# Kernel tuning notes

Measured on AMD Instinct MI355X. Metric: run time of the kernel, lower is better.

Reference implementation:

```python
import jax, jax.numpy as jnp
import numpy as np

NEG_SLOPE = 0.2  # PyG GATConv default negative_slope
NUM_GRAPHS = 64
N, E, F_IN = 50000, 800000, 128


def _gat(x, src, dst, W, a_s, a_d, b, concat):
    # PyG GATConv: h = x W (per head); e_ij = leaky_relu(a_s.h_j + a_d.h_i);
    # softmax over incoming edges of each dst node; out_i = sum_j alpha_ij h_j
    n = x.shape[0]
    H, C = a_s.shape
    h = (x @ W).reshape(n, H, C)                     # [N,H,C]
    es = jnp.einsum('nhc,hc->nh', h, a_s)            # [N,H]
    ed = jnp.einsum('nhc,hc->nh', h, a_d)
    e = jax.nn.leaky_relu(es[src] + ed[dst], NEG_SLOPE)   # [E,H]
    m = jax.ops.segment_max(e, dst, num_segments=n)       # per-dst max (stable softmax)
    ex = jnp.exp(e - m[dst])
    den = jax.ops.segment_sum(ex, dst, num_segments=n)
    alpha = ex / den[dst]                                 # [E,H]
    out = jax.ops.segment_sum(h[src] * alpha[:, :, None], dst, num_segments=n)  # [N,H,C]
    if concat:
        return out.reshape(n, H * C) + b
    return out.mean(axis=1) + b


def setup_inputs() -> dict:
    key = jax.random.key(0)
    ks = jax.random.split(key, 10)
    x = jax.random.normal(ks[0], (N, F_IN), jnp.float32)
    edge_index = jax.random.randint(ks[1], (2, E), 0, N, dtype=jnp.int64)
    batch = jnp.sort(jax.random.randint(ks[2], (N,), 0, NUM_GRAPHS, dtype=jnp.int64))
    s1 = 1.0 / np.sqrt(F_IN)
    s2 = 1.0 / np.sqrt(256)
    return {
        'x': x,
        'edge_index': edge_index,
        'batch': batch,
        'W1': jax.random.normal(ks[3], (F_IN, 256), jnp.float32) * s1,
        'a_src1': jax.random.normal(ks[4], (4, 64), jnp.float32) * s2,
        'a_dst1': jax.random.normal(ks[5], (4, 64), jnp.float32) * s2,
        'b1': jnp.zeros((256,), jnp.float32),
        'W2': jax.random.normal(ks[6], (256, 128), jnp.float32) * s2,
        'a_src2': jax.random.normal(ks[7], (1, 128), jnp.float32) * (1.0 / np.sqrt(128)),
        'a_dst2': jax.random.normal(ks[8], (1, 128), jnp.float32) * (1.0 / np.sqrt(128)),
        'b2': jnp.zeros((128,), jnp.float32),
        'fc_w': jax.random.normal(ks[9], (128, 10), jnp.float32) * (1.0 / np.sqrt(128)),
        'fc_b': jnp.zeros((10,), jnp.float32),
    }


def reference(x, edge_index, batch, W1, a_src1, a_dst1, b1, W2, a_src2, a_dst2, b2, fc_w, fc_b):
    n = x.shape[0]
    loop = jnp.arange(n, dtype=edge_index.dtype)  # PyG add_self_loops=True
    src = jnp.concatenate([edge_index[0], loop])
    dst = jnp.concatenate([edge_index[1], loop])
    h = jax.nn.elu(_gat(x, src, dst, W1, a_src1, a_dst1, b1, True))   # dropout: eval mode -> identity
    h = jax.nn.elu(_gat(h, src, dst, W2, a_src2, a_dst2, b2, False))
    pooled = jax.ops.segment_sum(h, batch, num_segments=NUM_GRAPHS)
    cnt = jax.ops.segment_sum(jnp.ones((n,), h.dtype), batch, num_segments=NUM_GRAPHS)
    pooled = pooled / jnp.maximum(cnt, 1.0)[:, None]
    logits = pooled @ fc_w + fc_b
    return jax.nn.log_softmax(logits, axis=1)
```

## Files before the change

kernel.cpp:

```cpp
#include <hip/hip_runtime.h>
#include <math.h>

#define N_NODES 50000
#define N_PAD   50048
#define N_EDGES 800000
#define E_TOT   (N_EDGES + N_NODES)
#define NG 64
#define CAP 48
#define NBKT 512
#define BNODES 98
#define RCAP 24
#define FILL_CHUNK 2048
#define GEMM1_BLOCKS 782
#define FILL_BLOCKS  391
#define PH1_TOTAL (GEMM1_BLOCKS + FILL_BLOCKS)
#define G2_NB 32

typedef short short8 __attribute__((ext_vector_type(8)));
typedef float floatx4 __attribute__((ext_vector_type(4)));
typedef float floatx2 __attribute__((ext_vector_type(2)));

__device__ inline short f2bf(float f) {
    union { float f; unsigned u; } v; v.f = f;
    unsigned r = v.u + 0x7fff + ((v.u >> 16) & 1);
    return (short)(r >> 16);
}

__device__ inline unsigned f2fp8(float f) {
    union { float f; unsigned u; } v; v.f = f;
    unsigned s = v.u & 0x80000000u;
    unsigned au = v.u & 0x7fffffffu;
    if (au > 0x43E00000u) au = 0x43E00000u;
    unsigned r = au + 0x7ffffu + ((au >> 20) & 1);
    int e8 = (int)(r >> 23) - 120;
    unsigned m3 = (r >> 20) & 7;
    unsigned code;
    if (e8 <= 0) code = 0;
    else if (e8 > 15) code = 0x7e;
    else code = ((unsigned)e8 << 3) | m3;
    return (s >> 24) | code;
}

__device__ inline float leaky_exp(float t) {
    t = t > 0.f ? t : 0.2f * t;
    return __expf(t);
}


__global__ __launch_bounds__(256) void phase1_kernel(const float* __restrict__ x,
                                                     const float* __restrict__ W1,
                                                     const float* __restrict__ a_s,
                                                     const float* __restrict__ a_d,
                                                     const int* __restrict__ ei,
                                                     unsigned short* __restrict__ gcnt,
                                                     unsigned* __restrict__ gb2,
                                                     unsigned char* __restrict__ C8,
                                                     float* __restrict__ es,
                                                     float* __restrict__ ed,
                                                     const float* __restrict__ W2,
                                                     const float* __restrict__ as2,
                                                     const float* __restrict__ ad2,
                                                     float* __restrict__ ws2,
                                                     float* __restrict__ wd2,
                                                     float* __restrict__ pooled) {
    __shared__ short bs[64][136];
    __shared__ int hist[NBKT];
    int bid = blockIdx.x;
    int tid = threadIdx.x;

    if (bid == PH1_TOTAL) {
        int k = tid;
        float s = 0.f, d = 0.f;
        for (int c = 0; c < 128; c++) {
            float w = W2[k * 128 + c];
            s += w * as2[c];
            d += w * ad2[c];
        }
        ws2[k] = s;
        wd2[k] = d;
        for (int i = tid; i < NG * 128; i += 256) pooled[i] = 0.f;
        return;
    }

    int gb = -1, fb = -1;
    {
        int g3 = bid / 3, r3 = bid - g3 * 3;
        if (r3 == 2) fb = g3;
        else         gb = g3 * 2 + r3;
    }

    if (fb >= 0) {
        hist[tid] = 0; hist[tid + 256] = 0;
        __syncthreads();
        unsigned meta[8], pay[8];
        int e0 = fb * FILL_CHUNK;
#pragma unroll
        for (int j = 0; j < 8; j++) {
            int t = e0 + j * 256 + tid;
            if (t < N_EDGES) {
                int s = ei[t];
                int d = ei[N_EDGES + t];
                unsigned bkt = (unsigned)d / 98u;
                int dlow = d - (int)bkt * 98;
                int pos = atomicAdd(&hist[bkt], 1);
                meta[j] = (bkt << 16) | (unsigned)pos;
                pay[j] = ((unsigned)s << 9) | (unsigned)dlow;
            } else {
                meta[j] = 0xffffffffu;
            }
        }
        __syncthreads();
        {
            int c0h = hist[tid];        if (c0h > RCAP) c0h = RCAP;
            int c1h = hist[tid + 256];  if (c1h > RCAP) c1h = RCAP;
            gcnt[fb * NBKT + tid] = (unsigned short)c0h;
            gcnt[fb * NBKT + tid + 256] = (unsigned short)c1h;
        }
#pragma unroll
        for (int j = 0; j < 8; j++) {
            if (meta[j] != 0xffffffffu) {
                unsigned bkt = meta[j] >> 16;
                unsigned pos = meta[j] & 0xffffu;
                if (pos < RCAP)
                    gb2[((size_t)bkt * FILL_BLOCKS + fb) * RCAP + pos] = pay[j];
            }
        }
        return;
    }

    const int K = 128, N = 256;
    int tc = tid & 63;
    int tk0s = (tid >> 6) * 32;
    int wid = tid >> 6;
    int lane = tid & 63;
    int m0 = gb * 64 + wid * 16;
    int mr = lane & 15;
    int quad = lane >> 4;
    int kq = quad << 3;
    int arow = m0 + mr; if (arow > N_NODES - 1) arow = N_NODES - 1;
    const float* aptr = x + (size_t)arow * K + kq;
    short8 a[4];
#pragma unroll
    for (int kk = 0; kk < 4; kk++) {
        float4 f0 = *(const float4*)(aptr + kk * 32);
        float4 f1 = *(const float4*)(aptr + kk * 32 + 4);
        a[kk][0] = f2bf(f0.x); a[kk][1] = f2bf(f0.y); a[kk][2] = f2bf(f0.z); a[kk][3] = f2bf(f0.w);
        a[kk][4] = f2bf(f1.x); a[kk][5] = f2bf(f1.y); a[kk][6] = f2bf(f1.z); a[kk][7] = f2bf(f1.w);
    }
    int orow = m0 + (quad << 2);
    for (int head = 0; head < 4; head++) {
        int c0 = head * 64;
        if (head) __syncthreads();
        for (int k = tk0s; k < tk0s + 32; k++)
            bs[tc][k] = f2bf(W1[k * 256 + c0 + tc]);
        __syncthreads();
        floatx4 acc[4] = {{0.f,0.f,0.f,0.f},{0.f,0.f,0.f,0.f},{0.f,0.f,0.f,0.f},{0.f,0.f,0.f,0.f}};
#pragma unroll
        for (int kk = 0; kk < 4; kk++) {
#pragma unroll
            for (int t = 0; t < 4; t++) {
                short8 b = *(const short8*)&bs[t * 16 + mr][kq + kk * 32];
                acc[t] = __builtin_amdgcn_mfma_f32_16x16x32_bf16(a[kk], b, acc[t], 0, 0, 0);
            }
        }
        float asv[4], adv[4];
#pragma unroll
        for (int t = 0; t < 4; t++) {
            asv[t] = a_s[c0 + t * 16 + mr];
            adv[t] = a_d[c0 + t * 16 + mr];
        }
#pragma unroll
        for (int r = 0; r < 4; r++) {
            float ps = acc[0][r] * asv[0] + acc[1][r] * asv[1] + acc[2][r] * asv[2] + acc[3][r] * asv[3];
            float pd = acc[0][r] * adv[0] + acc[1][r] * adv[1] + acc[2][r] * adv[2] + acc[3][r] * adv[3];
#pragma unroll
            for (int off = 8; off >= 1; off >>= 1) {
                ps += __shfl_xor(ps, off);
                pd += __shfl_xor(pd, off);
            }
            if (mr == 0) {
                es[(orow + r) * 4 + head] = ps;
                ed[(orow + r) * 4 + head] = pd;
            }
        }
#pragma unroll
        for (int t = 0; t < 4; t++) {
            int ocol = c0 + t * 16 + mr;
#pragma unroll
            for (int r = 0; r < 4; r++) {
                C8[(size_t)(orow + r) * N + ocol] = (unsigned char)f2fp8(acc[t][r]);
            }
        }
    }
}


__global__ __launch_bounds__(512) void binfill_kernel(const unsigned* __restrict__ gb2,
                                                      const unsigned short* __restrict__ gcnt,
                                                      unsigned short* __restrict__ col,
                                                      int* __restrict__ degT) {
    __shared__ unsigned colL[BNODES * CAP / 2];
    __shared__ int cnt[BNODES];
    __shared__ unsigned short cl[FILL_BLOCKS + 1];
    int b = blockIdx.x, tid = threadIdx.x;
    int nbase = b * BNODES;

    for (int i = tid; i < BNODES * CAP / 8; i += 512) ((uint4*)colL)[i] = make_uint4(0, 0, 0, 0);
    if (tid < FILL_BLOCKS) cl[tid] = gcnt[tid * NBKT + b];
    if (tid < BNODES) cnt[tid] = (nbase + tid < N_NODES) ? 1 : 0;
    __syncthreads();

    if (tid < BNODES) {
        int nn = nbase + tid;
        if (nn < N_NODES) ((unsigned short*)colL)[tid * CAP] = (unsigned short)nn;
    }
    const uint4* src4 = (const uint4*)(gb2 + (size_t)b * FILL_BLOCKS * RCAP);
    for (int r = tid; r < FILL_BLOCKS * RCAP / 4; r += 512) {
        int blk = r / 6;
        int q = r - blk * 6;
        int c = cl[blk];
        if (q * 4 < c) {
            uint4 v = src4[r];
            unsigned vv[4] = {v.x, v.y, v.z, v.w};
#pragma unroll
            for (int j = 0; j < 4; j++) {
                if (q * 4 + j < c) {
                    unsigned p = vv[j];
                    int dlow = (int)(p & 511u);
                    int s = (int)(p >> 9);
                    int sp = atomicAdd(&cnt[dlow], 1);
                    if (sp < CAP) ((unsigned short*)colL)[dlow * CAP + sp] = (unsigned short)s;
                }
            }
        }
    }
    __syncthreads();

    uint4* cb = (uint4*)(col + (size_t)b * BNODES * CAP);
    for (int i = tid; i < BNODES * CAP / 8; i += 512) cb[i] = ((uint4*)colL)[i];
    if (tid < BNODES) {
        int nn = nbase + tid;
        if (nn < N_NODES) degT[nn] = cnt[tid];
    }
}


__global__ __launch_bounds__(256) void gather1_kernel(const unsigned char* __restrict__ h8,
                                                      const int* __restrict__ degT,
                                                      const unsigned short* __restrict__ col,
                                                      const float* __restrict__ es,
                                                      const float* __restrict__ ed,
                                                      const float* __restrict__ bias,
                                                      const float* __restrict__ ws2,
                                                      const float* __restrict__ wd2,
                                                      short* __restrict__ out,
                                                      float* __restrict__ es2,
                                                      float* __restrict__ ed2) {
    __shared__ float wlds[4][CAP * 4];
    __shared__ unsigned short ilds[4][CAP];
    int tid = threadIdx.x;
    int wid = tid >> 6;
    int n = __builtin_amdgcn_readfirstlane(blockIdx.x * 4 + wid);
    int l = tid & 63;
    int hh = l >> 4;
    int cnt = degT[n]; cnt = cnt < CAP ? cnt : CAP;
    int cnt8 = (cnt + 7) & ~7;

    if (l < cnt8) ilds[wid][l] = col[n * CAP + l];

    {
        int eA = l >> 2;
        int hA = l & 3;
        float edvA = ed[n * 4 + hA];
#pragma unroll
        for (int p = 0; p < 3; p++) {
            int e = p * 16 + eA;
            if (e < cnt8) {
                int s = ilds[wid][e];
                float w = (e < cnt) ? leaky_exp(es[s * 4 + hA] + edvA) : 0.f;
                wlds[wid][e * 4 + hA] = w;
            }
        }
    }

    float ax = 0.f, ay = 0.f, az = 0.f, aw = 0.f, den = 0.f;
    for (int eb = 0; eb < cnt8; eb += 8) {
        int idx[8];
#pragma unroll
        for (int j = 0; j < 8; j++) idx[j] = ilds[wid][eb + j];
        float wv[8];
#pragma unroll
        for (int j = 0; j < 8; j++) wv[j] = wlds[wid][(eb + j) * 4 + hh];
        unsigned hv[8];
#pragma unroll
        for (int j = 0; j < 8; j++)
            hv[j] = *(const unsigned*)&h8[(size_t)idx[j] * 256 + l * 4];
#pragma unroll
        for (int j = 0; j < 8; j++) {
            floatx2 lo = __builtin_amdgcn_cvt_pk_f32_fp8(hv[j], false);
            floatx2 hi = __builtin_amdgcn_cvt_pk_f32_fp8(hv[j], true);
            den += wv[j];
            ax += wv[j] * lo[0];
            ay += wv[j] * lo[1];
            az += wv[j] * hi[0];
            aw += wv[j] * hi[1];
        }
    }
    float inv = 1.0f / den;
    float4 bb = *(const float4*)&bias[l * 4];
    float o0 = ax * inv + bb.x;
    float o1 = ay * inv + bb.y;
    float o2 = az * inv + bb.z;
    float o3 = aw * inv + bb.w;
    o0 = o0 > 0.f ? o0 : __expf(o0) - 1.f;
    o1 = o1 > 0.f ? o1 : __expf(o1) - 1.f;
    o2 = o2 > 0.f ? o2 : __expf(o2) - 1.f;
    o3 = o3 > 0.f ? o3 : __expf(o3) - 1.f;
    short4 ob;
    ob.x = f2bf(o0); ob.y = f2bf(o1); ob.z = f2bf(o2); ob.w = f2bf(o3);
    *(short4*)&out[(size_t)n * 256 + l * 4] = ob;

    float4 s4 = *(const float4*)&ws2[l * 4];
    float4 d4 = *(const float4*)&wd2[l * 4];
    float ps = o0 * s4.x + o1 * s4.y + o2 * s4.z + o3 * s4.w;
    float pd = o0 * d4.x + o1 * d4.y + o2 * d4.z + o3 * d4.w;
#pragma unroll
    for (int off = 32; off >= 1; off >>= 1) {
        ps += __shfl_xor(ps, off);
        pd += __shfl_xor(pd, off);
    }
    if (l == 0) {
        es2[n] = ps;
        ed2[n] = pd;
    }
}


__global__ __launch_bounds__(256) void gemm2_kernel(const short* __restrict__ A,
                                                    const float* __restrict__ W2,
                                                    unsigned char* __restrict__ C8) {
    __shared__ short bs[64][264];
    const int K = 256, N = 128;
    int tid = threadIdx.x;
    int tc = tid & 63;
    int tk0s = (tid >> 6) * 64;
    int wid = tid >> 6;
    int lane = tid & 63;
    int m0 = blockIdx.x * 64 + wid * 16;
    int mr = lane & 15;
    int quad = lane >> 4;
    int kq = quad << 3;
    const short* arow = A + (size_t)(m0 + mr) * K + kq;
    short8 a[8];
#pragma unroll
    for (int kk = 0; kk < 8; kk++) a[kk] = *(const short8*)(arow + kk * 32);
    int orow = m0 + (quad << 2);
    for (int by = 0; by < 2; by++) {
        int c0 = by * 64;
        if (by) __syncthreads();
        for (int k = tk0s; k < tk0s + 64; k++)
            bs[tc][k] = f2bf(W2[k * 128 + c0 + tc]);
        __syncthreads();
        floatx4 acc[4] = {{0.f,0.f,0.f,0.f},{0.f,0.f,0.f,0.f},{0.f,0.f,0.f,0.f},{0.f,0.f,0.f,0.f}};
#pragma unroll
        for (int kk = 0; kk < 8; kk++) {
#pragma unroll
            for (int t = 0; t < 4; t++) {
                short8 b = *(const short8*)&bs[t * 16 + mr][kq + kk * 32];
                acc[t] = __builtin_amdgcn_mfma_f32_16x16x32_bf16(a[kk], b, acc[t], 0, 0, 0);
            }
        }
#pragma unroll
        for (int t = 0; t < 4; t++) {
            int ocol = c0 + t * 16 + mr;
#pragma unroll
            for (int r = 0; r < 4; r++) {
                C8[(size_t)(orow + r) * N + ocol] = (unsigned char)f2fp8(acc[t][r]);
            }
        }
    }
}


__global__ __launch_bounds__(256) void gather2_kernel(const unsigned char* __restrict__ h8,
                                                      const int* __restrict__ deg,
                                                      const unsigned short* __restrict__ col,
                                                      const float* __restrict__ es2,
                                                      const float* __restrict__ ed2,
                                                      const float* __restrict__ bias,
                                                      const int* __restrict__ batch,
                                                      float* __restrict__ pooled) {
    __shared__ float wlds[4][CAP];
    __shared__ float plds[8][128];
    __shared__ int pg[8];
    __shared__ int pcnt;
    int tid = threadIdx.x;
    int wid = tid >> 6;
    int l = tid & 63;
    if (tid == 0) pcnt = 0;
    __syncthreads();

    int c0 = l * 2;
    float2 bb = *(const float2*)&bias[c0];
    int nbase = blockIdx.x * G2_NB + wid * (G2_NB / 4);
    int curg = -1;
    float a0 = 0.f, a1 = 0.f;

    auto flush = [&]() {
        if (curg >= 0) {
            int idx = 0;
            if (l == 0) idx = atomicAdd(&pcnt, 1);
            idx = __shfl(idx, 0);
            if (idx < 8) {
                if (l == 0) pg[idx] = curg;
                plds[idx][c0] = a0;
                plds[idx][c0 + 1] = a1;
            } else {
                atomicAdd(&pooled[curg * 128 + c0], a0);
                atomicAdd(&pooled[curg * 128 + c0 + 1], a1);
            }
        }
    };

    for (int i = 0; i < G2_NB / 4; i++) {
        int n = nbase + i;
        if (n < N_NODES) {
            int bg = batch[n];
            if (bg != curg) {
                flush();
                curg = bg; a0 = 0.f; a1 = 0.f;
            }
            int cnt = deg[n]; cnt = cnt < CAP ? cnt : CAP;
            int cnt8 = (cnt + 7) & ~7;
            float edv = ed2[n];
            if (l < cnt8) {
                int s = col[n * CAP + l];
                float w = (l < cnt) ? leaky_exp(es2[s] + edv) : 0.f;
                wlds[wid][l] = w;
            }
            const unsigned int* cp = (const unsigned int*)(col + n * CAP);
            float ax = 0.f, ay = 0.f, den = 0.f;
            for (int eb = 0; eb < cnt8; eb += 8) {
                unsigned int cw0 = cp[(eb >> 1) + 0];
                unsigned int cw1 = cp[(eb >> 1) + 1];
                unsigned int cw2 = cp[(eb >> 1) + 2];
                unsigned int cw3 = cp[(eb >> 1) + 3];
                int idx[8];
                idx[0] = cw0 & 0xffff; idx[1] = cw0 >> 16;
                idx[2] = cw1 & 0xffff; idx[3] = cw1 >> 16;
                idx[4] = cw2 & 0xffff; idx[5] = cw2 >> 16;
                idx[6] = cw3 & 0xffff; idx[7] = cw3 >> 16;
                float wv[8];
#pragma unroll
                for (int j = 0; j < 8; j++) wv[j] = wlds[wid][eb + j];
                unsigned hv[8];
#pragma unroll
                for (int j = 0; j < 8; j++)
                    hv[j] = *(const unsigned short*)&h8[(size_t)idx[j] * 128 + l * 2];
#pragma unroll
                for (int j = 0; j < 8; j++) {
                    floatx2 lo = __builtin_amdgcn_cvt_pk_f32_fp8(hv[j], false);
                    den += wv[j];
                    ax += wv[j] * lo[0];
                    ay += wv[j] * lo[1];
                }
            }
            float inv = 1.0f / den;
            float o0 = ax * inv + bb.x;
            float o1 = ay * inv + bb.y;
            o0 = o0 > 0.f ? o0 : __expf(o0) - 1.f;
            o1 = o1 > 0.f ? o1 : __expf(o1) - 1.f;
            a0 += o0; a1 += o1;
        }
    }
    flush();
    __syncthreads();

    int m = pcnt; if (m > 8) m = 8;
    if (tid < 128) {
        for (int e = 0; e < m; e++) {
            int ge = pg[e];
            bool first = true;
            for (int e2 = 0; e2 < e; e2++) if (pg[e2] == ge) first = false;
            if (first) {
                float s = plds[e][tid];
                for (int e3 = e + 1; e3 < m; e3++) if (pg[e3] == ge) s += plds[e3][tid];
                atomicAdd(&pooled[ge * 128 + tid], s);
            }
        }
    }
}


__global__ void fc_kernel(const float* __restrict__ pooled, const int* __restrict__ batch,
                          const float* __restrict__ fcw, const float* __restrict__ fcb,
                          float* __restrict__ out) {
    int g = threadIdx.x;
    if (g >= NG) return;
    int lo = 0, hi = N_NODES;
    while (lo < hi) {
        int mid = (lo + hi) >> 1;
        if (batch[mid] < g) lo = mid + 1; else hi = mid;
    }
    int start = lo;
    lo = start; hi = N_NODES;
    while (lo < hi) {
        int mid = (lo + hi) >> 1;
        if (batch[mid] <= g) lo = mid + 1; else hi = mid;
    }
    int cnt = lo - start;
    float inv = 1.0f / (float)(cnt > 0 ? cnt : 1);

    float lg[10];
#pragma unroll
    for (int j = 0; j < 10; j++) lg[j] = fcb[j];
    for (int k = 0; k < 128; k++) {
        float p = pooled[g * 128 + k] * inv;
#pragma unroll
        for (int j = 0; j < 10; j++) lg[j] += p * fcw[k * 10 + j];
    }
    float m = lg[0];
#pragma unroll
    for (int j = 1; j < 10; j++) m = fmaxf(m, lg[j]);
    float se = 0.f;
#pragma unroll
    for (int j = 0; j < 10; j++) se += __expf(lg[j] - m);
    float lse = m + __logf(se);
#pragma unroll
    for (int j = 0; j < 10; j++) out[g * 10 + j] = lg[j] - lse;
}


extern "C" void kernel_launch(void* const* d_in, const int* in_sizes, int n_in,
                              void* d_out, int out_size, void* d_ws, size_t ws_size,
                              hipStream_t stream) {
    const float* x     = (const float*)d_in[0];
    const int*   ei    = (const int*)d_in[1];
    const int*   batch = (const int*)d_in[2];
    const float* W1    = (const float*)d_in[3];
    const float* as1   = (const float*)d_in[4];
    const float* ad1   = (const float*)d_in[5];
    const float* b1    = (const float*)d_in[6];
    const float* W2    = (const float*)d_in[7];
    const float* as2   = (const float*)d_in[8];
    const float* ad2   = (const float*)d_in[9];
    const float* b2    = (const float*)d_in[10];
    const float* fcw   = (const float*)d_in[11];
    const float* fcb   = (const float*)d_in[12];
    float* out = (float*)d_out;

    char* ws = (char*)d_ws;
    size_t off = 0;
    auto alloc = [&](size_t bytes) -> void* {
        void* p = ws + off;
        off = (off + bytes + 255) & ~(size_t)255;
        return p;
    };
    float* pooled        = (float*)alloc(NG * 128 * 4);
    int* degT            = (int*)alloc((size_t)N_PAD * 4);
    unsigned short* col  = (unsigned short*)alloc((size_t)NBKT * BNODES * CAP * 2);
    unsigned* gb2        = (unsigned*)alloc((size_t)NBKT * FILL_BLOCKS * RCAP * 4);
    unsigned short* gcnt = (unsigned short*)alloc((size_t)FILL_BLOCKS * NBKT * 2);
    float* es1           = (float*)alloc((size_t)N_PAD * 4 * 4);
    float* ed1           = (float*)alloc((size_t)N_PAD * 4 * 4);
    float* es2           = (float*)alloc((size_t)N_PAD * 4);
    float* ed2           = (float*)alloc((size_t)N_PAD * 4);
    float* ws2           = (float*)alloc(256 * 4);
    float* wd2           = (float*)alloc(256 * 4);
    unsigned char* h1    = (unsigned char*)alloc((size_t)N_PAD * 256);
    short* h1p           = (short*)alloc((size_t)N_PAD * 256 * 2);
    unsigned char* h2    = (unsigned char*)alloc((size_t)N_PAD * 128);

    phase1_kernel<<<PH1_TOTAL + 1, 256, 0, stream>>>(x, W1, as1, ad1, ei, gcnt, gb2, h1, es1, ed1,
                                                     W2, as2, ad2, ws2, wd2, pooled);
    binfill_kernel<<<NBKT, 512, 0, stream>>>(gb2, gcnt, col, degT);
    gather1_kernel<<<N_NODES / 4, 256, 0, stream>>>(h1, degT, col, es1, ed1, b1, ws2, wd2,
                                                    h1p, es2, ed2);
    gemm2_kernel<<<N_PAD / 64, 256, 0, stream>>>(h1p, W2, h2);
    gather2_kernel<<<(N_NODES + G2_NB - 1) / G2_NB, 256, 0, stream>>>(h2, degT, col, es2, ed2, b2,
                                                                      batch, pooled);
    fc_kernel<<<1, 64, 0, stream>>>(pooled, batch, fcw, fcb, out);
}
```

Baseline: 231.8 us.

## Software-pipeline gather kernels with 16-edge batches and drop LDS weight staging

Both GAT gather kernels drop the LDS staging of neighbor indices and attention weights. Each lane now reads packed column indices directly as uint4 and computes the leaky-exp weight inline from gathered es values. Edges are handled in 16-wide batches with double-buffered registers, so the loads for the next batch are issued before the current one is consumed, which should hide gather latency. Gather2 also processes fewer nodes per block to raise the block count. In exchange, register pressure rises and the exp work is repeated per lane instead of being shared.

```diff
diff --git a/kernel.cpp b/kernel.cpp
--- a/kernel.cpp
+++ b/kernel.cpp
@@ -14,7 +14,7 @@
 #define GEMM1_BLOCKS 782
 #define FILL_BLOCKS  391
 #define PH1_TOTAL (GEMM1_BLOCKS + FILL_BLOCKS)
-#define G2_NB 32
+#define G2_NB 16
 
 typedef short short8 __attribute__((ext_vector_type(8)));
 typedef float floatx4 __attribute__((ext_vector_type(4)));
@@ -256,56 +256,58 @@
                                                       short* __restrict__ out,
                                                       float* __restrict__ es2,
                                                       float* __restrict__ ed2) {
-    __shared__ float wlds[4][CAP * 4];
-    __shared__ unsigned short ilds[4][CAP];
     int tid = threadIdx.x;
     int wid = tid >> 6;
     int n = __builtin_amdgcn_readfirstlane(blockIdx.x * 4 + wid);
     int l = tid & 63;
     int hh = l >> 4;
     int cnt = degT[n]; cnt = cnt < CAP ? cnt : CAP;
-    int cnt8 = (cnt + 7) & ~7;
-
-    if (l < cnt8) ilds[wid][l] = col[n * CAP + l];
-
-    {
-        int eA = l >> 2;
-        int hA = l & 3;
-        float edvA = ed[n * 4 + hA];
-#pragma unroll
-        for (int p = 0; p < 3; p++) {
-            int e = p * 16 + eA;
-            if (e < cnt8) {
-                int s = ilds[wid][e];
-                float w = (e < cnt) ? leaky_exp(es[s * 4 + hA] + edvA) : 0.f;
-                wlds[wid][e * 4 + hA] = w;
-            }
-        }
-    }
+
+    const uint4* cp4 = (const uint4*)(col + n * CAP);
+    float edv = ed[n * 4 + hh];
 
     float ax = 0.f, ay = 0.f, az = 0.f, aw = 0.f, den = 0.f;
-    for (int eb = 0; eb < cnt8; eb += 8) {
-        int idx[8];
-#pragma unroll
-        for (int j = 0; j < 8; j++) idx[j] = ilds[wid][eb + j];
-        float wv[8];
-#pragma unroll
-        for (int j = 0; j < 8; j++) wv[j] = wlds[wid][(eb + j) * 4 + hh];
-        unsigned hv[8];
-#pragma unroll
-        for (int j = 0; j < 8; j++)
-            hv[j] = *(const unsigned*)&h8[(size_t)idx[j] * 256 + l * 4];
-#pragma unroll
-        for (int j = 0; j < 8; j++) {
-            floatx2 lo = __builtin_amdgcn_cvt_pk_f32_fp8(hv[j], false);
-            floatx2 hi = __builtin_amdgcn_cvt_pk_f32_fp8(hv[j], true);
-            den += wv[j];
-            ax += wv[j] * lo[0];
-            ay += wv[j] * lo[1];
-            az += wv[j] * hi[0];
-            aw += wv[j] * hi[1];
-        }
-    }
+    unsigned hv0[16], hv1[16];
+    float ev0[16], ev1[16];
+    unsigned ids[16];
+
+#define G1_UNPACK(eb) { \
+    uint4 ca = cp4[(eb) >> 3]; uint4 cb = cp4[((eb) >> 3) + 1]; \
+    ids[0]  = ca.x & 0xffffu;  ids[1]  = ca.x >> 16; \
+    ids[2]  = ca.y & 0xffffu;  ids[3]  = ca.y >> 16; \
+    ids[4]  = ca.z & 0xffffu;  ids[5]  = ca.z >> 16; \
+    ids[6]  = ca.w & 0xffffu;  ids[7]  = ca.w >> 16; \
+    ids[8]  = cb.x & 0xffffu;  ids[9]  = cb.x >> 16; \
+    ids[10] = cb.y & 0xffffu;  ids[11] = cb.y >> 16; \
+    ids[12] = cb.z & 0xffffu;  ids[13] = cb.z >> 16; \
+    ids[14] = cb.w & 0xffffu;  ids[15] = cb.w >> 16; }
+
+#define G1_ISSUE(hv, ev) { \
+    _Pragma("unroll") \
+    for (int j = 0; j < 16; j++) hv[j] = *(const unsigned*)&h8[(size_t)ids[j] * 256 + l * 4]; \
+    _Pragma("unroll") \
+    for (int j = 0; j < 16; j++) ev[j] = es[ids[j] * 4 + hh]; }
+
+#define G1_CONS(eb, hv, ev) { \
+    _Pragma("unroll") \
+    for (int j = 0; j < 16; j++) { \
+        float w = ((eb) + j < cnt) ? leaky_exp(ev[j] + edv) : 0.f; \
+        floatx2 lo = __builtin_amdgcn_cvt_pk_f32_fp8(hv[j], false); \
+        floatx2 hi = __builtin_amdgcn_cvt_pk_f32_fp8(hv[j], true); \
+        den += w; ax += w * lo[0]; ay += w * lo[1]; az += w * hi[0]; aw += w * hi[1]; } }
+
+    G1_UNPACK(0); G1_ISSUE(hv0, ev0);
+    if (cnt > 16) { G1_UNPACK(16); G1_ISSUE(hv1, ev1); }
+    G1_CONS(0, hv0, ev0);
+    if (cnt > 16) {
+        if (cnt > 32) { G1_UNPACK(32); G1_ISSUE(hv0, ev0); }
+        G1_CONS(16, hv1, ev1);
+        if (cnt > 32) G1_CONS(32, hv0, ev0);
+    }
+#undef G1_UNPACK
+#undef G1_ISSUE
+#undef G1_CONS
+
     float inv = 1.0f / den;
     float4 bb = *(const float4*)&bias[l * 4];
     float o0 = ax * inv + bb.x;
@@ -390,7 +392,6 @@
                                                       const float* __restrict__ bias,
                                                       const int* __restrict__ batch,
                                                       float* __restrict__ pooled) {
-    __shared__ float wlds[4][CAP];
     __shared__ float plds[8][128];
     __shared__ int pg[8];
     __shared__ int pcnt;
@@ -422,6 +423,34 @@
         }
     };
 
+    unsigned hv0[16], hv1[16];
+    float ev0[16], ev1[16];
+    unsigned ids[16];
+
+#define G2_UNPACK(cp4, eb) { \
+    uint4 ca = cp4[(eb) >> 3]; uint4 cb = cp4[((eb) >> 3) + 1]; \
+    ids[0]  = ca.x & 0xffffu;  ids[1]  = ca.x >> 16; \
+    ids[2]  = ca.y & 0xffffu;  ids[3]  = ca.y >> 16; \
+    ids[4]  = ca.z & 0xffffu;  ids[5]  = ca.z >> 16; \
+    ids[6]  = ca.w & 0xffffu;  ids[7]  = ca.w >> 16; \
+    ids[8]  = cb.x & 0xffffu;  ids[9]  = cb.x >> 16; \
+    ids[10] = cb.y & 0xffffu;  ids[11] = cb.y >> 16; \
+    ids[12] = cb.z & 0xffffu;  ids[13] = cb.z >> 16; \
+    ids[14] = cb.w & 0xffffu;  ids[15] = cb.w >> 16; }
+
+#define G2_ISSUE(hv, ev) { \
+    _Pragma("unroll") \
+    for (int j = 0; j < 16; j++) hv[j] = *(const unsigned short*)&h8[(size_t)ids[j] * 128 + l * 2]; \
+    _Pragma("unroll") \
+    for (int j = 0; j < 16; j++) ev[j] = es2[ids[j]]; }
+
+#define G2_CONS(eb, hv, ev) { \
+    _Pragma("unroll") \
+    for (int j = 0; j < 16; j++) { \
+        float w = ((eb) + j < cnt) ? leaky_exp(ev[j] + ed2v) : 0.f; \
+        floatx2 lo = __builtin_amdgcn_cvt_pk_f32_fp8(hv[j], false); \
+        den += w; ax += w * lo[0]; ay += w * lo[1]; } }
+
     for (int i = 0; i < G2_NB / 4; i++) {
         int n = nbase + i;
         if (n < N_NODES) {
@@ -431,40 +460,19 @@
                 curg = bg; a0 = 0.f; a1 = 0.f;
             }
             int cnt = deg[n]; cnt = cnt < CAP ? cnt : CAP;
-            int cnt8 = (cnt + 7) & ~7;
-            float edv = ed2[n];
-            if (l < cnt8) {
-                int s = col[n * CAP + l];
-                float w = (l < cnt) ? leaky_exp(es2[s] + edv) : 0.f;
-                wlds[wid][l] = w;
-            }
-            const unsigned int* cp = (const unsigned int*)(col + n * CAP);
+            const uint4* cp4 = (const uint4*)(col + n * CAP);
+            float ed2v = ed2[n];
             float ax = 0.f, ay = 0.f, den = 0.f;
-            for (int eb = 0; eb < cnt8; eb += 8) {
-                unsigned int cw0 = cp[(eb >> 1) + 0];
-                unsigned int cw1 = cp[(eb >> 1) + 1];
-                unsigned int cw2 = cp[(eb >> 1) + 2];
-                unsigned int cw3 = cp[(eb >> 1) + 3];
-                int idx[8];
-                idx[0] = cw0 & 0xffff; idx[1] = cw0 >> 16;
-                idx[2] = cw1 & 0xffff; idx[3] = cw1 >> 16;
-                idx[4] = cw2 & 0xffff; idx[5] = cw2 >> 16;
-                idx[6] = cw3 & 0xffff; idx[7] = cw3 >> 16;
-                float wv[8];
-#pragma unroll
-                for (int j = 0; j < 8; j++) wv[j] = wlds[wid][eb + j];
-                unsigned hv[8];
-#pragma unroll
-                for (int j = 0; j < 8; j++)
-                    hv[j] = *(const unsigned short*)&h8[(size_t)idx[j] * 128 + l * 2];
-#pragma unroll
-                for (int j = 0; j < 8; j++) {
-                    floatx2 lo = __builtin_amdgcn_cvt_pk_f32_fp8(hv[j], false);
-                    den += wv[j];
-                    ax += wv[j] * lo[0];
-                    ay += wv[j] * lo[1];
-                }
-            }
+
+            G2_UNPACK(cp4, 0); G2_ISSUE(hv0, ev0);
+            if (cnt > 16) { G2_UNPACK(cp4, 16); G2_ISSUE(hv1, ev1); }
+            G2_CONS(0, hv0, ev0);
+            if (cnt > 16) {
+                if (cnt > 32) { G2_UNPACK(cp4, 32); G2_ISSUE(hv0, ev0); }
+                G2_CONS(16, hv1, ev1);
+                if (cnt > 32) G2_CONS(32, hv0, ev0);
+            }
+
             float inv = 1.0f / den;
             float o0 = ax * inv + bb.x;
             float o1 = ay * inv + bb.y;
@@ -473,6 +481,9 @@
             a0 += o0; a1 += o1;
         }
     }
+#undef G2_UNPACK
+#undef G2_ISSUE
+#undef G2_CONS
     flush();
     __syncthreads();
 
```

Measured after the change: 268.9 us. 1.16x slower.
